# Optimization experiments

Hardware: AMD Instinct MI355X
Metric: run time of the kernel (lower is better)

Reference implementation:

```python
import jax, jax.numpy as jnp
import numpy as np


def _log_exp_kernel(x):
    # positive feature map log(1 + exp(x)) (softplus), per the kernel's name
    return jax.nn.softplus(x)


def setup_inputs() -> dict:
    key0 = jax.random.key(0)
    ks = jax.random.split(key0, 8)
    N, L, H, d = 2, 2048, 8, 64
    D = H * d
    s = 1.0 / np.sqrt(D)
    return {
        "query": jax.random.normal(ks[0], (N, L, D), jnp.float32),
        "key": jax.random.normal(ks[1], (N, L, D), jnp.float32),
        "Wq": jax.random.normal(ks[2], (D, D), jnp.float32) * s,
        "Wk": jax.random.normal(ks[3], (D, D), jnp.float32) * s,
        "Wv": jax.random.normal(ks[4], (D, D), jnp.float32) * s,
        "position_coeffs": jax.random.normal(ks[5], (H, d), jnp.float32),
        "position_weight": jax.random.normal(ks[6], (H, d, 1), jnp.float32) * 0.02,
        "position_bias": jax.random.normal(ks[7], (H, d), jnp.float32) * 0.02,
    }


def reference(query, key, Wq, Wk, Wv, position_coeffs, position_weight, position_bias):
    N, Lq, D = query.shape
    Lk = key.shape[1]
    H, d, P = position_weight.shape

    # default positions: arange, P=1 (broadcast over batch)
    qpos = jnp.arange(Lq, dtype=query.dtype).reshape(1, Lq, 1)  # (1, Lq, P)

    # projections + kernel feature map; (N, H, L, d)
    q = _log_exp_kernel((query @ Wq.T).reshape(N, Lq, H, d)).transpose(0, 2, 1, 3)
    k = _log_exp_kernel((key @ Wk.T).reshape(N, Lk, H, d)).transpose(0, 2, 1, 3)
    v = (key @ Wv.T).reshape(N, Lk, H, d).transpose(0, 2, 1, 3)

    # projected positions; NOTE: source uses query_positions for pk too (faithful)
    pq = jnp.einsum('nlp,hkp->nhlk', qpos, position_weight) + position_bias[None, :, None, :]
    pk = jnp.einsum('nlp,hkp->nhlk', qpos, position_weight)  # (1, H, Lq, d)

    coeff = position_coeffs[None, :, None, :]  # (1, H, 1, d)
    cos_a = q * jnp.cos(pq)
    cos_b = coeff * k * jnp.cos(pk)
    sin_a = q * jnp.sin(pq)
    sin_b = coeff * k * jnp.sin(pk)

    # (N, H, Lq, Lk) quadratic score
    score = (jnp.einsum('nhqd,nhkd->nhqk', cos_a, cos_b)
             + jnp.einsum('nhqd,nhkd->nhqk', sin_a, sin_b))

    # future mask (future_offset = 0): zero out keys j > query i
    future = jnp.arange(Lk)[None, :] > jnp.arange(Lq)[:, None]
    score = jnp.where(future[None, None], jnp.zeros((), score.dtype), score)

    # scaled: rows sum (in abs) to 1
    score = score / jnp.sum(jnp.abs(score), axis=-1, keepdims=True)

    att = jnp.einsum('nhqk,nhkd->nhqd', score, v)
    return att.transpose(0, 2, 1, 3).reshape(N, Lq, D)
```

## Files before the change

### kernel.cpp

```cpp
#include <hip/hip_runtime.h>
#include <hip/hip_bf16.h>
#include <cstdint>


typedef __bf16 bf16x8 __attribute__((ext_vector_type(8)));
typedef float f32x16 __attribute__((ext_vector_type(16)));
typedef unsigned short u16x8 __attribute__((ext_vector_type(8)));

__device__ __forceinline__ unsigned short f2bfu(float f) {
    uint32_t u = __float_as_uint(f);
    uint32_t r = (u + 0x7fffu + ((u >> 16) & 1u)) >> 16;
    return (unsigned short)r;
}
__device__ __forceinline__ uint32_t cvt2(float a, float b) {
    __hip_bfloat162 h = __float22bfloat162_rn(make_float2(a, b));
    return *reinterpret_cast<uint32_t*>(&h);
}
__device__ __forceinline__ float softplusf(float x) {
    return fmaxf(x, 0.f) + __logf(1.f + __expf(-fabsf(x)));
}

__global__ __launch_bounds__(256) void cvt_kernel(
    const float* __restrict__ query, const float* __restrict__ key,
    const float* __restrict__ Wq, const float* __restrict__ Wk,
    const float* __restrict__ Wv,
    unsigned short* __restrict__ Xqb, unsigned short* __restrict__ Xkb,
    unsigned short* __restrict__ Wqb, unsigned short* __restrict__ Wkb,
    unsigned short* __restrict__ Wvb)
{
    const int z = blockIdx.z;
    const float* src;
    unsigned short* dst;
    int n8;
    if (z == 0)      { src = query; dst = Xqb; n8 = 4096 * 512 / 8; }
    else if (z == 1) { src = key;   dst = Xkb; n8 = 4096 * 512 / 8; }
    else if (z == 2) { src = Wq;    dst = Wqb; n8 = 512 * 512 / 8;  }
    else if (z == 3) { src = Wk;    dst = Wkb; n8 = 512 * 512 / 8;  }
    else             { src = Wv;    dst = Wvb; n8 = 512 * 512 / 8;  }
    int idx = blockIdx.x * 256 + threadIdx.x;
    if (idx >= n8) return;
    const float4* s = (const float4*)src + (size_t)idx * 2;
    float4 a = s[0], b = s[1];
    uint4 o;
    o.x = cvt2(a.x, a.y); o.y = cvt2(a.z, a.w);
    o.z = cvt2(b.x, b.y); o.w = cvt2(b.z, b.w);
    *(uint4*)&dst[(size_t)idx * 8] = o;
}

__global__ __launch_bounds__(256) void proj_kernel(
    const unsigned short* __restrict__ Xqb, const unsigned short* __restrict__ Xkb,
    const unsigned short* __restrict__ Wqb, const unsigned short* __restrict__ Wkb,
    const unsigned short* __restrict__ Wvb, const float* __restrict__ coef,
    const float* __restrict__ posw, const float* __restrict__ posb,
    unsigned short* __restrict__ Af, unsigned short* __restrict__ Bf,
    unsigned short* __restrict__ Vf)
{
    const int mode = blockIdx.z;
    const int c0 = blockIdx.x * 128;
    const int m0 = blockIdx.y * 128;
    const unsigned short* X = (mode == 0) ? Xqb : Xkb;
    const unsigned short* W = (mode == 0) ? Wqb : (mode == 1 ? Wkb : Wvb);

    __shared__ __align__(16) char smem[128 * 72 * 2 * 2];
    unsigned short* Xs = (unsigned short*)smem;
    unsigned short* Ws = (unsigned short*)(smem + 128 * 72 * 2);

    const int t = threadIdx.x;
    const int lane = t & 63, wv = t >> 6;
    const int lm = lane & 31, half = lane >> 5;
    const int wrow = wv >> 1, wcol = wv & 1;

    f32x16 acc[2][2] = {};

    u16x8 px[4], pw[4];
    {
#pragma unroll
        for (int it = 0; it < 4; ++it) {
            int cid = t + it * 256, row = cid >> 3, seg = cid & 7;
            px[it] = *(const u16x8*)&X[(size_t)(m0 + row) * 512 + seg * 8];
            pw[it] = *(const u16x8*)&W[(size_t)(c0 + row) * 512 + seg * 8];
        }
    }

    for (int kt = 0; kt < 8; ++kt) {
        __syncthreads();
#pragma unroll
        for (int it = 0; it < 4; ++it) {
            int cid = t + it * 256, row = cid >> 3, seg = cid & 7;
            *(u16x8*)&Xs[row * 72 + seg * 8] = px[it];
            *(u16x8*)&Ws[row * 72 + seg * 8] = pw[it];
        }
        __syncthreads();
        if (kt < 7) {
            int ko = (kt + 1) * 64;
#pragma unroll
            for (int it = 0; it < 4; ++it) {
                int cid = t + it * 256, row = cid >> 3, seg = cid & 7;
                px[it] = *(const u16x8*)&X[(size_t)(m0 + row) * 512 + ko + seg * 8];
                pw[it] = *(const u16x8*)&W[(size_t)(c0 + row) * 512 + ko + seg * 8];
            }
        }
        const unsigned short* ab = &Xs[(64 * wrow + lm) * 72 + half * 8];
        const unsigned short* bb = &Ws[(64 * wcol + lm) * 72 + half * 8];
        __builtin_amdgcn_s_setprio(1);
#pragma unroll
        for (int ks = 0; ks < 4; ++ks) {
            bf16x8 a0 = *(const bf16x8*)(ab + ks * 16);
            bf16x8 a1 = *(const bf16x8*)(ab + 32 * 72 + ks * 16);
            bf16x8 b0 = *(const bf16x8*)(bb + ks * 16);
            bf16x8 b1 = *(const bf16x8*)(bb + 32 * 72 + ks * 16);
            acc[0][0] = __builtin_amdgcn_mfma_f32_32x32x16_bf16(a0, b0, acc[0][0], 0, 0, 0);
            acc[0][1] = __builtin_amdgcn_mfma_f32_32x32x16_bf16(a0, b1, acc[0][1], 0, 0, 0);
            acc[1][0] = __builtin_amdgcn_mfma_f32_32x32x16_bf16(a1, b0, acc[1][0], 0, 0, 0);
            acc[1][1] = __builtin_amdgcn_mfma_f32_32x32x16_bf16(a1, b1, acc[1][1], 0, 0, 0);
        }
        __builtin_amdgcn_s_setprio(0);
    }

    if (mode != 2) {
        unsigned short* Feat = (mode == 0) ? Af : Bf;
#pragma unroll
        for (int i = 0; i < 2; ++i)
#pragma unroll
        for (int j = 0; j < 2; ++j)
#pragma unroll
        for (int r = 0; r < 16; ++r) {
            int rl = (r & 3) + 8 * (r >> 2) + 4 * half;
            int m = m0 + 64 * wrow + 32 * i + rl;
            int c = c0 + 64 * wcol + 32 * j + lm;
            int n = m >> 11, l = m & 2047;
            int h = c >> 6, jj = c & 63;
            float ang = (float)l * posw[c] + ((mode == 0) ? posb[c] : 0.f);
            float sn, cs; __sincosf(ang, &sn, &cs);
            float v = softplusf(acc[i][j][r]);
            if (mode == 1) v *= coef[c];
            size_t base = ((size_t)(n * 8 + h) * 2048 + l) * 128 + jj;
            Feat[base]      = f2bfu(v * cs);
            Feat[base + 64] = f2bfu(v * sn);
        }
    } else {
        float* tb = (float*)smem;
        float* tbw = tb + wv * (32 * 34);
        __syncthreads();
#pragma unroll
        for (int i = 0; i < 2; ++i)
#pragma unroll
        for (int j = 0; j < 2; ++j) {
#pragma unroll
            for (int r = 0; r < 16; ++r) {
                int rl = (r & 3) + 8 * (r >> 2) + 4 * half;
                tbw[lm * 34 + rl] = acc[i][j][r];
            }
            int mb = m0 + 64 * wrow + 32 * i;
            int n = mb >> 11, l0 = mb & 2047;
#pragma unroll
            for (int rep = 0; rep < 16; ++rep) {
                int cl = rep * 2 + half;
                float v = tbw[cl * 34 + lm];
                int c = c0 + 64 * wcol + 32 * j + cl;
                int h = c >> 6, dd = c & 63;
                Vf[((size_t)(n * 8 + h) * 64 + dd) * 2048 + l0 + lm] = f2bfu(v);
            }
        }
    }
}

__global__ __launch_bounds__(256) void attn_kernel(
    const unsigned short* __restrict__ Af, const unsigned short* __restrict__ Bf,
    const unsigned short* __restrict__ Vf, float* __restrict__ out)
{
    const int bx = blockIdx.x;
    const int nh = bx & 15;
    const int p  = bx >> 4;
    const int qq = (p < 16) ? p : 47 - p;
    const int q0 = qq * 64;

    __shared__ unsigned short Bs[64 * 136];
    __shared__ unsigned short Ss[64 * 72];
    __shared__ unsigned short Vs[64 * 72];
    __shared__ float zf[64];

    const int t = threadIdx.x;
    const int lane = t & 63, wv = t >> 6;
    const int lm = lane & 31, half = lane >> 5;
    const int wrow = wv >> 1, wcol = wv & 1;
    const int n = nh >> 3, h = nh & 7;

    const unsigned short* Ah = Af + (size_t)nh * 2048 * 128;
    const unsigned short* Bh = Bf + (size_t)nh * 2048 * 128;
    const unsigned short* Vh = Vf + (size_t)nh * 64 * 2048;

#pragma unroll
    for (int it = 0; it < 4; ++it) {
        int cid = t + it * 256, row = cid >> 4, off = (cid & 15) << 3;
        *(u16x8*)&Bs[row * 136 + off] = *(const u16x8*)&Ah[(size_t)(q0 + row) * 128 + off];
    }
    if (t < 64) zf[t] = 0.f;
    __syncthreads();
    bf16x8 afrag[8];
    {
        const unsigned short* ab = &Bs[(32 * wrow + lm) * 136 + half * 8];
#pragma unroll
        for (int c = 0; c < 8; ++c) afrag[c] = *(const bf16x8*)(ab + c * 16);
    }

    f32x16 oacc = {};
    float zp[16];
#pragma unroll
    for (int r = 0; r < 16; ++r) zp[r] = 0.f;

    u16x8 pb[4], pv[2];
#pragma unroll
    for (int it = 0; it < 4; ++it) {
        int cid = t + it * 256, row = cid >> 4, off = (cid & 15) << 3;
        pb[it] = *(const u16x8*)&Bh[(size_t)row * 128 + off];
    }
#pragma unroll
    for (int it = 0; it < 2; ++it) {
        int cid = t + it * 256, row = cid >> 3, off = (cid & 7) << 3;
        pv[it] = *(const u16x8*)&Vh[(size_t)row * 2048 + off];
    }

    for (int kt = 0; kt <= qq; ++kt) {
        __syncthreads();
#pragma unroll
        for (int it = 0; it < 4; ++it) {
            int cid = t + it * 256, row = cid >> 4, off = (cid & 15) << 3;
            *(u16x8*)&Bs[row * 136 + off] = pb[it];
        }
#pragma unroll
        for (int it = 0; it < 2; ++it) {
            int cid = t + it * 256, row = cid >> 3, off = (cid & 7) << 3;
            *(u16x8*)&Vs[row * 72 + off] = pv[it];
        }
        __syncthreads();
        if (kt < qq) {
            int k1 = (kt + 1) * 64;
#pragma unroll
            for (int it = 0; it < 4; ++it) {
                int cid = t + it * 256, row = cid >> 4, off = (cid & 15) << 3;
                pb[it] = *(const u16x8*)&Bh[(size_t)(k1 + row) * 128 + off];
            }
#pragma unroll
            for (int it = 0; it < 2; ++it) {
                int cid = t + it * 256, row = cid >> 3, off = (cid & 7) << 3;
                pv[it] = *(const u16x8*)&Vh[(size_t)row * 2048 + k1 + off];
            }
        }

        f32x16 sacc = {};
        const unsigned short* bbase = &Bs[(32 * wcol + lm) * 136 + half * 8];
        __builtin_amdgcn_s_setprio(1);
#pragma unroll
        for (int ks = 0; ks < 8; ++ks) {
            bf16x8 b = *(const bf16x8*)(bbase + ks * 16);
            sacc = __builtin_amdgcn_mfma_f32_32x32x16_bf16(afrag[ks], b, sacc, 0, 0, 0);
        }
        __builtin_amdgcn_s_setprio(0);
        if (kt == qq) {
#pragma unroll
            for (int r = 0; r < 16; ++r) {
                int rl = (r & 3) + 8 * (r >> 2) + 4 * half;
                if ((32 * wcol + lm) > (32 * wrow + rl)) sacc[r] = 0.f;
            }
        }
#pragma unroll
        for (int r = 0; r < 16; ++r) zp[r] += fabsf(sacc[r]);

#pragma unroll
        for (int r = 0; r < 16; ++r) {
            int rl = (r & 3) + 8 * (r >> 2) + 4 * half;
            Ss[(32 * wrow + rl) * 72 + 32 * wcol + lm] = f2bfu(sacc[r]);
        }
        __syncthreads();

        const unsigned short* sbase = &Ss[(32 * wrow + lm) * 72 + half * 8];
        const unsigned short* vbase = &Vs[(32 * wcol + lm) * 72 + half * 8];
        __builtin_amdgcn_s_setprio(1);
#pragma unroll
        for (int kc = 0; kc < 4; ++kc) {
            bf16x8 a = *(const bf16x8*)(sbase + kc * 16);
            bf16x8 b = *(const bf16x8*)(vbase + kc * 16);
            oacc = __builtin_amdgcn_mfma_f32_32x32x16_bf16(a, b, oacc, 0, 0, 0);
        }
        __builtin_amdgcn_s_setprio(0);
    }

    __syncthreads();
#pragma unroll
    for (int r = 0; r < 16; ++r) {
        float z = zp[r];
        z += __shfl_xor(z, 1);
        z += __shfl_xor(z, 2);
        z += __shfl_xor(z, 4);
        z += __shfl_xor(z, 8);
        z += __shfl_xor(z, 16);
        if (lm == 0) {
            int rl = (r & 3) + 8 * (r >> 2) + 4 * half;
            atomicAdd(&zf[32 * wrow + rl], z);
        }
    }
    __syncthreads();
#pragma unroll
    for (int r = 0; r < 16; ++r) {
        int rl = (r & 3) + 8 * (r >> 2) + 4 * half;
        int q = q0 + 32 * wrow + rl;
        float invz = 1.f / zf[32 * wrow + rl];
        out[((size_t)(n * 2048 + q)) * 512 + h * 64 + 32 * wcol + lm] = oacc[r] * invz;
    }
}

extern "C" void kernel_launch(void* const* d_in, const int* in_sizes, int n_in,
                              void* d_out, int out_size, void* d_ws, size_t ws_size,
                              hipStream_t stream) {
    (void)in_sizes; (void)n_in; (void)out_size; (void)ws_size;
    const float* query = (const float*)d_in[0];
    const float* key   = (const float*)d_in[1];
    const float* Wq    = (const float*)d_in[2];
    const float* Wk    = (const float*)d_in[3];
    const float* Wv    = (const float*)d_in[4];
    const float* coef  = (const float*)d_in[5];
    const float* posw  = (const float*)d_in[6];
    const float* posb  = (const float*)d_in[7];

    unsigned short* Af  = (unsigned short*)d_ws;
    unsigned short* Bf  = Af + (size_t)16 * 2048 * 128;
    unsigned short* Vf  = Bf + (size_t)16 * 2048 * 128;
    unsigned short* Xqb = Vf + (size_t)16 * 64 * 2048;
    unsigned short* Xkb = Xqb + (size_t)4096 * 512;
    unsigned short* Wqb = Xkb + (size_t)4096 * 512;
    unsigned short* Wkb = Wqb + (size_t)512 * 512;
    unsigned short* Wvb = Wkb + (size_t)512 * 512;

    cvt_kernel<<<dim3(1024, 1, 5), 256, 0, stream>>>(
        query, key, Wq, Wk, Wv, Xqb, Xkb, Wqb, Wkb, Wvb);
    proj_kernel<<<dim3(4, 32, 3), 256, 0, stream>>>(
        Xqb, Xkb, Wqb, Wkb, Wvb, coef, posw, posb, Af, Bf, Vf);
    attn_kernel<<<dim3(512), 256, 0, stream>>>(
        Af, Bf, Vf, (float*)d_out);
}
```

Baseline: 143.0 us.

## Keep attention scores in registers via transposed QK and permlane swap

The score tile is now computed transposed (K as A operand, Q as B operand), so each lane holds one query's scores across keys. The lanes then pack them to bf16 and use v_permlane32_swap to form the A operand for the PV MFMA directly. This removes the LDS round trip for scores and one barrier per key tile, and the row-sum reduction becomes a per-lane accumulation. In exchange each wave covers a 32-key slice for all 64 head dims with two accumulators, so a cross-wave reduction of partial outputs through LDS is added at the end.

```diff
diff --git a/kernel.cpp b/kernel.cpp
--- a/kernel.cpp
+++ b/kernel.cpp
@@ -6,6 +6,7 @@
 typedef __bf16 bf16x8 __attribute__((ext_vector_type(8)));
 typedef float f32x16 __attribute__((ext_vector_type(16)));
 typedef unsigned short u16x8 __attribute__((ext_vector_type(8)));
+typedef uint32_t u32x4 __attribute__((ext_vector_type(4)));
 
 __device__ __forceinline__ unsigned short f2bfu(float f) {
     uint32_t u = __float_as_uint(f);
@@ -18,6 +19,14 @@
 }
 __device__ __forceinline__ float softplusf(float x) {
     return fmaxf(x, 0.f) + __logf(1.f + __expf(-fabsf(x)));
+}
+__device__ __forceinline__ uint32_t pkbf(float a, float b) {
+    uint32_t d;
+    asm("v_cvt_pk_bf16_f32 %0, %1, %2" : "=v"(d) : "v"(a), "v"(b));
+    return d;
+}
+__device__ __forceinline__ void plswap(uint32_t& a, uint32_t& b) {
+    asm volatile("v_permlane32_swap_b32 %0, %1" : "+v"(a), "+v"(b));
 }
 
 __global__ __launch_bounds__(256) void cvt_kernel(
@@ -176,14 +185,13 @@
     const int q0 = qq * 64;
 
     __shared__ unsigned short Bs[64 * 136];
-    __shared__ unsigned short Ss[64 * 72];
     __shared__ unsigned short Vs[64 * 72];
     __shared__ float zf[64];
 
     const int t = threadIdx.x;
     const int lane = t & 63, wv = t >> 6;
     const int lm = lane & 31, half = lane >> 5;
-    const int wrow = wv >> 1, wcol = wv & 1;
+    const int qb = wv >> 1, kb = wv & 1;
     const int n = nh >> 3, h = nh & 7;
 
     const unsigned short* Ah = Af + (size_t)nh * 2048 * 128;
@@ -197,17 +205,15 @@
     }
     if (t < 64) zf[t] = 0.f;
     __syncthreads();
-    bf16x8 afrag[8];
+    bf16x8 qfrag[8];
     {
-        const unsigned short* ab = &Bs[(32 * wrow + lm) * 136 + half * 8];
-#pragma unroll
-        for (int c = 0; c < 8; ++c) afrag[c] = *(const bf16x8*)(ab + c * 16);
-    }
-
-    f32x16 oacc = {};
-    float zp[16];
-#pragma unroll
-    for (int r = 0; r < 16; ++r) zp[r] = 0.f;
+        const unsigned short* ab = &Bs[(32 * qb + lm) * 136 + half * 8];
+#pragma unroll
+        for (int c = 0; c < 8; ++c) qfrag[c] = *(const bf16x8*)(ab + c * 16);
+    }
+
+    f32x16 oacc0 = {}, oacc1 = {};
+    float zsum = 0.f;
 
     u16x8 pb[4], pv[2];
 #pragma unroll
@@ -249,64 +255,84 @@
         }
 
         f32x16 sacc = {};
-        const unsigned short* bbase = &Bs[(32 * wcol + lm) * 136 + half * 8];
+        const unsigned short* kbase = &Bs[(32 * kb + lm) * 136 + half * 8];
         __builtin_amdgcn_s_setprio(1);
 #pragma unroll
         for (int ks = 0; ks < 8; ++ks) {
-            bf16x8 b = *(const bf16x8*)(bbase + ks * 16);
-            sacc = __builtin_amdgcn_mfma_f32_32x32x16_bf16(afrag[ks], b, sacc, 0, 0, 0);
+            bf16x8 kf = *(const bf16x8*)(kbase + ks * 16);
+            sacc = __builtin_amdgcn_mfma_f32_32x32x16_bf16(kf, qfrag[ks], sacc, 0, 0, 0);
         }
         __builtin_amdgcn_s_setprio(0);
+
         if (kt == qq) {
 #pragma unroll
             for (int r = 0; r < 16; ++r) {
-                int rl = (r & 3) + 8 * (r >> 2) + 4 * half;
-                if ((32 * wcol + lm) > (32 * wrow + rl)) sacc[r] = 0.f;
-            }
-        }
-#pragma unroll
-        for (int r = 0; r < 16; ++r) zp[r] += fabsf(sacc[r]);
-
+                int kl = (r & 3) + 8 * (r >> 2) + 4 * half;
+                if ((32 * kb + kl) > (32 * qb + lm)) sacc[r] = 0.f;
+            }
+        }
+#pragma unroll
+        for (int r = 0; r < 16; ++r) zsum += fabsf(sacc[r]);
+
+        union { u32x4 u; bf16x8 b; } pa0, pa1;
+        {
+            uint32_t A = pkbf(sacc[0], sacc[1]);
+            uint32_t B = pkbf(sacc[2], sacc[3]);
+            uint32_t C = pkbf(sacc[4], sacc[5]);
+            uint32_t D = pkbf(sacc[6], sacc[7]);
+            plswap(A, C);
+            plswap(B, D);
+            pa0.u = (u32x4){A, B, C, D};
+            uint32_t E = pkbf(sacc[8], sacc[9]);
+            uint32_t F = pkbf(sacc[10], sacc[11]);
+            uint32_t G = pkbf(sacc[12], sacc[13]);
+            uint32_t H = pkbf(sacc[14], sacc[15]);
+            plswap(E, G);
+            plswap(F, H);
+            pa1.u = (u32x4){E, F, G, H};
+        }
+
+        const unsigned short* v0 = &Vs[(size_t)lm * 72 + 32 * kb + half * 8];
+        const unsigned short* v1 = &Vs[(size_t)(32 + lm) * 72 + 32 * kb + half * 8];
+        __builtin_amdgcn_s_setprio(1);
+        {
+            bf16x8 vb00 = *(const bf16x8*)(v0);
+            bf16x8 vb10 = *(const bf16x8*)(v1);
+            oacc0 = __builtin_amdgcn_mfma_f32_32x32x16_bf16(pa0.b, vb00, oacc0, 0, 0, 0);
+            oacc1 = __builtin_amdgcn_mfma_f32_32x32x16_bf16(pa0.b, vb10, oacc1, 0, 0, 0);
+            bf16x8 vb01 = *(const bf16x8*)(v0 + 16);
+            bf16x8 vb11 = *(const bf16x8*)(v1 + 16);
+            oacc0 = __builtin_amdgcn_mfma_f32_32x32x16_bf16(pa1.b, vb01, oacc0, 0, 0, 0);
+            oacc1 = __builtin_amdgcn_mfma_f32_32x32x16_bf16(pa1.b, vb11, oacc1, 0, 0, 0);
+        }
+        __builtin_amdgcn_s_setprio(0);
+    }
+
+    atomicAdd(&zf[32 * qb + lm], zsum);
+    __syncthreads();
+
+    float* Os = (float*)Bs;
+    if (kb == 0) {
 #pragma unroll
         for (int r = 0; r < 16; ++r) {
-            int rl = (r & 3) + 8 * (r >> 2) + 4 * half;
-            Ss[(32 * wrow + rl) * 72 + 32 * wcol + lm] = f2bfu(sacc[r]);
-        }
-        __syncthreads();
-
-        const unsigned short* sbase = &Ss[(32 * wrow + lm) * 72 + half * 8];
-        const unsigned short* vbase = &Vs[(32 * wcol + lm) * 72 + half * 8];
-        __builtin_amdgcn_s_setprio(1);
-#pragma unroll
-        for (int kc = 0; kc < 4; ++kc) {
-            bf16x8 a = *(const bf16x8*)(sbase + kc * 16);
-            bf16x8 b = *(const bf16x8*)(vbase + kc * 16);
-            oacc = __builtin_amdgcn_mfma_f32_32x32x16_bf16(a, b, oacc, 0, 0, 0);
-        }
-        __builtin_amdgcn_s_setprio(0);
-    }
-
+            int ql = (r & 3) + 8 * (r >> 2) + 4 * half;
+            Os[(32 * qb + ql) * 65 + lm]      = oacc0[r];
+            Os[(32 * qb + ql) * 65 + 32 + lm] = oacc1[r];
+        }
+    }
     __syncthreads();
-#pragma unroll
-    for (int r = 0; r < 16; ++r) {
-        float z = zp[r];
-        z += __shfl_xor(z, 1);
-        z += __shfl_xor(z, 2);
-        z += __shfl_xor(z, 4);
-        z += __shfl_xor(z, 8);
-        z += __shfl_xor(z, 16);
-        if (lm == 0) {
-            int rl = (r & 3) + 8 * (r >> 2) + 4 * half;
-            atomicAdd(&zf[32 * wrow + rl], z);
-        }
-    }
-    __syncthreads();
-#pragma unroll
-    for (int r = 0; r < 16; ++r) {
-        int rl = (r & 3) + 8 * (r >> 2) + 4 * half;
-        int q = q0 + 32 * wrow + rl;
-        float invz = 1.f / zf[32 * wrow + rl];
-        out[((size_t)(n * 2048 + q)) * 512 + h * 64 + 32 * wcol + lm] = oacc[r] * invz;
+    if (kb == 1) {
+#pragma unroll
+        for (int r = 0; r < 16; ++r) {
+            int ql = (r & 3) + 8 * (r >> 2) + 4 * half;
+            int q = q0 + 32 * qb + ql;
+            float invz = 1.f / zf[32 * qb + ql];
+            float o0 = (Os[(32 * qb + ql) * 65 + lm]      + oacc0[r]) * invz;
+            float o1 = (Os[(32 * qb + ql) * 65 + 32 + lm] + oacc1[r]) * invz;
+            size_t base = ((size_t)(n * 2048 + q)) * 512 + h * 64;
+            out[base + lm]      = o0;
+            out[base + 32 + lm] = o1;
+        }
     }
 }
 
```

New measurement: 133.0 us. -7.0%, faster.
